# Optimization experiments

Hardware: AMD Instinct MI355X
Metric: run time of the kernel (lower is better)

Reference implementation:

```python
import jax, jax.numpy as jnp
import numpy as np

B, T, C, H = 4, 2048, 1024, 16
HD = C // H  # head_dim = 64


def setup_inputs() -> dict:
    key = jax.random.key(0)
    k1, k2, k3 = jax.random.split(key, 3)
    x = jax.random.normal(k1, (B, T, C), dtype=jnp.float32)
    # nn.Linear weights are [out, in]; we store transposed [in, out] for x @ W
    w_qkv = jax.random.normal(k2, (C, 3 * C), dtype=jnp.float32) * (1.0 / np.sqrt(C))
    w_proj = jax.random.normal(k3, (C, C), dtype=jnp.float32) * (1.0 / np.sqrt(C))
    return {"x": x, "w_qkv": w_qkv, "w_proj": w_proj}


def reference(x, w_qkv, w_proj):
    Bs, Ts, Cs = x.shape
    qkv = x @ w_qkv  # [B,T,3C]
    q, k, v = jnp.split(qkv, 3, axis=-1)

    def split_heads(t):
        return t.reshape(Bs, Ts, H, HD).transpose(0, 2, 1, 3)  # [B,H,T,HD]

    q, k, v = split_heads(q), split_heads(k), split_heads(v)
    scale = 1.0 / np.sqrt(HD)
    scores = jnp.einsum('bhqd,bhkd->bhqk', q, k) * scale  # [B,H,T,T]
    causal = jnp.tril(jnp.ones((Ts, Ts), dtype=bool))
    scores = jnp.where(causal, scores, -jnp.inf)
    weights = jax.nn.softmax(scores, axis=-1)
    out = jnp.einsum('bhqk,bhkd->bhqd', weights, v)  # [B,H,T,HD]
    out = out.transpose(0, 2, 1, 3).reshape(Bs, Ts, Cs)
    return out @ w_proj
```

## Files before the change

kernel.cpp:

```cpp
#include <hip/hip_runtime.h>
#include <stdint.h>


typedef __attribute__((ext_vector_type(8))) short bf16x8;
typedef __attribute__((ext_vector_type(4))) float f32x4;

#define MFMA(a, b, c) __builtin_amdgcn_mfma_f32_16x16x32_bf16((a), (b), (c), 0, 0, 0)

#define NB 4
#define NT 2048
#define NC 1024
#define NH 16
#define HD 64
#define SCALE_Q 0.18033688011112042f

__device__ __forceinline__ short f2bf(float f) {
  union { float fv; uint32_t u; } v; v.fv = f;
  uint32_t u = v.u;
  uint32_t r = (u + 0x7fffu + ((u >> 16) & 1u)) >> 16;
  return (short)(r & 0xffffu);
}

__device__ __forceinline__ uint32_t pkbf(float a, float b) {
  union { float f; uint32_t u; } ua, ub; ua.f = a; ub.f = b;
  return __builtin_amdgcn_perm(ub.u + 0x8000u, ua.u + 0x8000u, 0x07060302u);
}

__device__ __forceinline__ void gl_lds16(const void* g, void* l) {
  __builtin_amdgcn_global_load_lds(
      (const __attribute__((address_space(1))) void*)g,
      (__attribute__((address_space(3))) void*)l, 16, 0, 0);
}


__global__ void cast_f32_bf16(const float* __restrict__ src, short* __restrict__ dst, int n8) {
  int i = blockIdx.x * blockDim.x + threadIdx.x;
  if (i >= n8) return;
  const float4* s4 = (const float4*)src;
  float4 a = s4[2 * i], b = s4[2 * i + 1];
  bf16x8 o;
  o[0] = f2bf(a.x); o[1] = f2bf(a.y); o[2] = f2bf(a.z); o[3] = f2bf(a.w);
  o[4] = f2bf(b.x); o[5] = f2bf(b.y); o[6] = f2bf(b.z); o[7] = f2bf(b.w);
  *(bf16x8*)&dst[8 * i] = o;
}

__global__ void transpose_cast(const float* __restrict__ src, short* __restrict__ dst,
                               int R, int Cc) {
  __shared__ float tile[64][65];
  int tid = threadIdx.x;
  int c0 = blockIdx.x * 64;
  int r0 = blockIdx.y * 64;
  int lr = tid >> 4;
  int lc = (tid & 15) * 4;
#pragma unroll
  for (int i = 0; i < 4; i++) {
    int rr = lr + i * 16;
    float4 v = *(const float4*)&src[(size_t)(r0 + rr) * Cc + c0 + lc];
    tile[rr][lc + 0] = v.x; tile[rr][lc + 1] = v.y;
    tile[rr][lc + 2] = v.z; tile[rr][lc + 3] = v.w;
  }
  __syncthreads();
  int oc = tid >> 2;
  int seg = (tid & 3) * 16;
  bf16x8 o0, o1;
#pragma unroll
  for (int u = 0; u < 8; u++) o0[u] = f2bf(tile[seg + u][oc]);
#pragma unroll
  for (int u = 0; u < 8; u++) o1[u] = f2bf(tile[seg + 8 + u][oc]);
  size_t base = (size_t)(c0 + oc) * R + r0 + seg;
  *(bf16x8*)&dst[base] = o0;
  *(bf16x8*)&dst[base + 8] = o1;
}


__global__ __launch_bounds__(256, 2)
void gemm_bt_kernel(const short* __restrict__ A, const short* __restrict__ BT,
                    int N, int K, int nbx, int mode,
                    short* __restrict__ q, short* __restrict__ kk, short* __restrict__ vT,
                    float* __restrict__ f_out) {
  __shared__ short sA[128 * 64];
  __shared__ short sB[128 * 64];
  const int tid = threadIdx.x;
  const int lane = tid & 63;
  const int w = tid >> 6;
  const int quad = lane >> 4;
  const int r = lane & 15;

  const int bid = blockIdx.x;
  const int xcd = bid & 7;
  const int local = bid >> 3;
  const int mloc = local / nbx, nloc = local - mloc * nbx;
  const int bm0 = (xcd * 8 + mloc) * 128;
  const int bn0 = nloc * 128;

  const int wm = (w >> 1) * 64;
  const int wn = (w & 1) * 64;
  const int sel = (mode == 0) ? (bn0 >> 10) : 3;
  const bool swapped = (sel != 2);

  f32x4 acc[4][4];
#pragma unroll
  for (int i = 0; i < 4; i++)
#pragma unroll
    for (int j = 0; j < 4; j++) acc[i][j] = (f32x4){0.f, 0.f, 0.f, 0.f};

  for (int kb = 0; kb < K; kb += 64) {
    __syncthreads();
#pragma unroll
    for (int j2 = 0; j2 < 4; j2++) {
      int idx = (w * 4 + j2) * 64 + lane;
      int row = idx >> 3, ch = idx & 7;
      int g = ch ^ (row & 7);
      gl_lds16(A + (size_t)(bm0 + row) * K + kb + g * 8, (char*)sA + idx * 16);
      gl_lds16(BT + (size_t)(bn0 + row) * K + kb + g * 8, (char*)sB + idx * 16);
    }
    __syncthreads();
#pragma unroll
    for (int c = 0; c < 2; c++) {
      bf16x8 af[4], bfr[4];
#pragma unroll
      for (int i = 0; i < 4; i++) {
        const int sw = ((c << 2) + quad) ^ (r & 7);
        af[i]  = *(const bf16x8*)&sA[(wm + i * 16 + r) * 64 + sw * 8];
        bfr[i] = *(const bf16x8*)&sB[(wn + i * 16 + r) * 64 + sw * 8];
      }
      if (swapped) {
#pragma unroll
        for (int i = 0; i < 4; i++)
#pragma unroll
          for (int j = 0; j < 4; j++)
            acc[i][j] = MFMA(bfr[j], af[i], acc[i][j]);
      } else {
#pragma unroll
        for (int i = 0; i < 4; i++)
#pragma unroll
          for (int j = 0; j < 4; j++)
            acc[i][j] = MFMA(af[i], bfr[j], acc[i][j]);
      }
    }
  }

  if (mode == 1) {
#pragma unroll
    for (int i = 0; i < 4; i++) {
      const int m = bm0 + wm + i * 16 + r;
#pragma unroll
      for (int j = 0; j < 4; j++) {
        const int nf = bn0 + wn + j * 16 + quad * 4;
        *(f32x4*)&f_out[(size_t)m * N + nf] = acc[i][j];
      }
    }
  } else if (sel == 2) {
#pragma unroll
    for (int j = 0; j < 4; j++) {
      const int n = bn0 + wn + j * 16 + r;
      const int d = n & 63, h = (n & 1023) >> 6;
#pragma unroll
      for (int i = 0; i < 4; i++) {
        const int t0 = bm0 + wm + i * 16 + quad * 4;
        const int bh = (t0 >> 11) * NH + h;
        uint2 pk = make_uint2(pkbf(acc[i][j][0], acc[i][j][1]),
                              pkbf(acc[i][j][2], acc[i][j][3]));
        *(uint2*)&vT[((size_t)bh * HD + d) * NT + (t0 & 2047)] = pk;
      }
    }
  } else {
    short* dst = (sel == 0) ? q : kk;
    const float scl = (sel == 0) ? SCALE_Q : 1.0f;
#pragma unroll
    for (int i = 0; i < 4; i++) {
      const int t = bm0 + wm + i * 16 + r;
      const int bb = (t >> 11) * NH;
      const int tt = t & 2047;
#pragma unroll
      for (int j = 0; j < 4; j++) {
        const int nf = bn0 + wn + j * 16 + quad * 4;
        const int rem = nf & 1023, h = rem >> 6, d0 = rem & 63;
        uint2 pk = make_uint2(pkbf(acc[i][j][0] * scl, acc[i][j][1] * scl),
                              pkbf(acc[i][j][2] * scl, acc[i][j][3] * scl));
        *(uint2*)&dst[((size_t)(bb + h) * NT + tt) * HD + d0] = pk;
      }
    }
  }
}


__device__ __forceinline__ void attn_band(
    const short* __restrict__ Qb, const short* __restrict__ Kb,
    const short* __restrict__ VTb, short* __restrict__ Og,
    short* __restrict__ sK, short* __restrict__ sV, short* __restrict__ sPw,
    const int band, const int bh, const int w, const int lane) {
  const int quad = lane >> 4;
  const int r = lane & 15;
  const int q0 = band * 128 + w * 32;

  bf16x8 bQ[2][2];
#pragma unroll
  for (int mi = 0; mi < 2; mi++) {
    const size_t qrow = ((size_t)q0 + mi * 16 + r) * HD;
    bQ[mi][0] = *(const bf16x8*)&Qb[qrow + quad * 8];
    bQ[mi][1] = *(const bf16x8*)&Qb[qrow + 32 + quad * 8];
  }
  bf16x8 vone;
#pragma unroll
  for (int u = 0; u < 8; u++) vone[u] = (short)0x3F80;

  f32x4 acc[2][4];
  f32x4 lacc[2];
#pragma unroll
  for (int mi = 0; mi < 2; mi++) {
    lacc[mi] = (f32x4){0.f, 0.f, 0.f, 0.f};
#pragma unroll
    for (int dt = 0; dt < 4; dt++) acc[mi][dt] = (f32x4){0.f, 0.f, 0.f, 0.f};
  }

  for (int kt = 0; kt <= band; kt++) {
    const int kv0 = kt * 128;
    const bool diag = (kt == band);
    __syncthreads();
#pragma unroll
    for (int j = 0; j < 4; j++) {
      int idx = (w * 4 + j) * 64 + lane;
      int krow = idx >> 3, kch = idx & 7;
      int kg = kch ^ (krow & 7);
      gl_lds16(Kb + (size_t)(kv0 + krow) * HD + kg * 8, (char*)sK + idx * 16);
      int vrow = idx >> 4, vch = idx & 15;
      int vg = (vch & 8) | ((vch ^ vrow) & 7);
      gl_lds16(VTb + (size_t)vrow * NT + kv0 + vg * 8, (char*)sV + idx * 16);
    }
    __syncthreads();

    bf16x8 vf[4][4];
#pragma unroll
    for (int dt = 0; dt < 4; dt++)
#pragma unroll
      for (int c = 0; c < 4; c++) {
        int ch = quad + 4 * c;
        int sw = (ch & 8) | ((ch ^ (r & 7)) & 7);
        vf[dt][c] = *(const bf16x8*)&sV[(dt * 16 + r) * 128 + sw * 8];
      }

#pragma unroll
    for (int mi = 0; mi < 2; mi++) {
      const int nts = diag ? (w * 2 + mi + 1) : 8;
#pragma unroll
      for (int nt = 0; nt < 8; nt++) {
        uint2 pk = make_uint2(0u, 0u);
        if (nt < nts) {
          const int krow = nt * 16 + r;
          const int sw0 = quad ^ (r & 7);
          bf16x8 k0 = *(const bf16x8*)&sK[krow * 64 + sw0 * 8];
          bf16x8 k1 = *(const bf16x8*)&sK[krow * 64 + (sw0 ^ 4) * 8];
          f32x4 st = (f32x4){0.f, 0.f, 0.f, 0.f};
          st = MFMA(k0, bQ[mi][0], st);
          st = MFMA(k1, bQ[mi][1], st);
          if (diag && nt == nts - 1) {
            const int kvb = kv0 + nt * 16 + quad * 4;
            const int qg = q0 + mi * 16 + r;
#pragma unroll
            for (int reg = 0; reg < 4; reg++)
              if (kvb + reg > qg) st[reg] = -1e30f;
          }
          pk.x = pkbf(__builtin_amdgcn_exp2f(st[0]), __builtin_amdgcn_exp2f(st[1]));
          pk.y = pkbf(__builtin_amdgcn_exp2f(st[2]), __builtin_amdgcn_exp2f(st[3]));
        }
        *(uint2*)&sPw[r * 136 + nt * 16 + quad * 4] = pk;
      }
      __builtin_amdgcn_s_waitcnt(0xc07f);
      bf16x8 aP[4];
#pragma unroll
      for (int c = 0; c < 4; c++)
        aP[c] = *(const bf16x8*)&sPw[r * 136 + c * 32 + quad * 8];
#pragma unroll
      for (int c = 0; c < 4; c++)
        lacc[mi] = MFMA(aP[c], vone, lacc[mi]);
#pragma unroll
      for (int dt = 0; dt < 4; dt++)
#pragma unroll
        for (int c = 0; c < 4; c++)
          acc[mi][dt] = MFMA(aP[c], vf[dt][c], acc[mi][dt]);
    }
  }

  const int b = bh >> 4, h = bh & 15;
#pragma unroll
  for (int mi = 0; mi < 2; mi++)
#pragma unroll
    for (int reg = 0; reg < 4; reg++) {
      const int trow = q0 + mi * 16 + quad * 4 + reg;
      const float inv = 1.0f / lacc[mi][reg];
      const size_t base = ((size_t)(b * NT + trow)) * NC + h * HD;
#pragma unroll
      for (int dt = 0; dt < 4; dt++)
        Og[base + dt * 16 + r] = f2bf(acc[mi][dt][reg] * inv);
    }
}

__global__ __launch_bounds__(256, 3)
void attn_kernel(const short* __restrict__ Q, const short* __restrict__ Kg,
                 const short* __restrict__ VT, short* __restrict__ Og) {
  __shared__ short sK[128 * 64];
  __shared__ short sV[64 * 128];
  __shared__ short sP[4][16 * 136];
  const int tid = threadIdx.x;
  const int lane = tid & 63;
  const int w = tid >> 6;

  const int n = blockIdx.x;
  const int xcd = n & 7;
  const int slot = n >> 3;
  const int bh = xcd * 8 + (slot & 7);
  const int pr = slot >> 3;

  const short* Qb  = Q  + (size_t)bh * NT * HD;
  const short* Kb  = Kg + (size_t)bh * NT * HD;
  const short* VTb = VT + (size_t)bh * HD * NT;

  attn_band(Qb, Kb, VTb, Og, sK, sV, &sP[w][0], 15 - pr, bh, w, lane);
  attn_band(Qb, Kb, VTb, Og, sK, sV, &sP[w][0], pr, bh, w, lane);
}


extern "C" void kernel_launch(void* const* d_in, const int* in_sizes, int n_in,
                              void* d_out, int out_size, void* d_ws, size_t ws_size,
                              hipStream_t stream) {
  const float* x     = (const float*)d_in[0];
  const float* wqkv  = (const float*)d_in[1];
  const float* wproj = (const float*)d_in[2];
  float* out = (float*)d_out;

  char* ws = (char*)d_ws;
  short* xb  = (short*)(ws + 0);
  short* wqT = (short*)(ws + 16777216);
  short* wpT = (short*)(ws + 23068672);
  short* q   = (short*)(ws + 25165824);
  short* kk  = (short*)(ws + 41943040);
  short* vT  = (short*)(ws + 58720256);
  short* att = (short*)(ws + 75497472);

  cast_f32_bf16<<<4096, 256, 0, stream>>>(x, xb, (NB * NT * NC) / 8);
  transpose_cast<<<dim3(48, 16), 256, 0, stream>>>(wqkv, wqT, NC, 3 * NC);
  transpose_cast<<<dim3(16, 16), 256, 0, stream>>>(wproj, wpT, NC, NC);
  gemm_bt_kernel<<<1536, 256, 0, stream>>>(xb, wqT, 3 * NC, NC, 24, 0, q, kk, vT, nullptr);
  attn_kernel<<<512, 256, 0, stream>>>(q, kk, vT, att);
  gemm_bt_kernel<<<512, 256, 0, stream>>>(att, wpT, NC, NC, 8, 1, nullptr, nullptr, nullptr, out);
}
```

Baseline: 300.0 us.

## Launch one attention block per causal band and share K fragment loads across row tiles

The attention grid goes from 512 blocks, each doing a paired heavy and light causal band, to 1024 blocks that each do a single band. Heavy bands are dispatched first so the hardware scheduler can balance the uneven causal work. Inside each KV tile, the two 16-row query sub-tiles now share a single set of K fragment loads from LDS. The second sub-tile's packed probabilities are held in registers until the first sub-tile's PV MFMAs finish. This trims LDS reads and adds parallelism, at the cost of more register pressure and less explicit pairing of work per block.

Measured after the change: 274.7 us. -8.4%, faster.

```diff
diff --git a/kernel.cpp b/kernel.cpp
--- a/kernel.cpp
+++ b/kernel.cpp
@@ -240,45 +240,81 @@
         vf[dt][c] = *(const bf16x8*)&sV[(dt * 16 + r) * 128 + sw * 8];
       }
 
-#pragma unroll
-    for (int mi = 0; mi < 2; mi++) {
-      const int nts = diag ? (w * 2 + mi + 1) : 8;
-#pragma unroll
-      for (int nt = 0; nt < 8; nt++) {
-        uint2 pk = make_uint2(0u, 0u);
-        if (nt < nts) {
-          const int krow = nt * 16 + r;
-          const int sw0 = quad ^ (r & 7);
-          bf16x8 k0 = *(const bf16x8*)&sK[krow * 64 + sw0 * 8];
-          bf16x8 k1 = *(const bf16x8*)&sK[krow * 64 + (sw0 ^ 4) * 8];
+    const int nts0 = diag ? (w * 2 + 1) : 8;
+    const int nts1 = diag ? (w * 2 + 2) : 8;
+    uint2 pk1r[8];
+#pragma unroll
+    for (int nt = 0; nt < 8; nt++) {
+      uint2 pk0 = make_uint2(0u, 0u);
+      pk1r[nt] = make_uint2(0u, 0u);
+      if (nt < nts1) {
+        const int krow = nt * 16 + r;
+        const int sw0 = quad ^ (r & 7);
+        bf16x8 k0 = *(const bf16x8*)&sK[krow * 64 + sw0 * 8];
+        bf16x8 k1 = *(const bf16x8*)&sK[krow * 64 + (sw0 ^ 4) * 8];
+        if (nt < nts0) {
           f32x4 st = (f32x4){0.f, 0.f, 0.f, 0.f};
-          st = MFMA(k0, bQ[mi][0], st);
-          st = MFMA(k1, bQ[mi][1], st);
-          if (diag && nt == nts - 1) {
+          st = MFMA(k0, bQ[0][0], st);
+          st = MFMA(k1, bQ[0][1], st);
+          if (diag && nt == nts0 - 1) {
             const int kvb = kv0 + nt * 16 + quad * 4;
-            const int qg = q0 + mi * 16 + r;
+            const int qg = q0 + r;
 #pragma unroll
             for (int reg = 0; reg < 4; reg++)
               if (kvb + reg > qg) st[reg] = -1e30f;
           }
-          pk.x = pkbf(__builtin_amdgcn_exp2f(st[0]), __builtin_amdgcn_exp2f(st[1]));
-          pk.y = pkbf(__builtin_amdgcn_exp2f(st[2]), __builtin_amdgcn_exp2f(st[3]));
+          pk0.x = pkbf(__builtin_amdgcn_exp2f(st[0]), __builtin_amdgcn_exp2f(st[1]));
+          pk0.y = pkbf(__builtin_amdgcn_exp2f(st[2]), __builtin_amdgcn_exp2f(st[3]));
         }
-        *(uint2*)&sPw[r * 136 + nt * 16 + quad * 4] = pk;
-      }
-      __builtin_amdgcn_s_waitcnt(0xc07f);
+        {
+          f32x4 st = (f32x4){0.f, 0.f, 0.f, 0.f};
+          st = MFMA(k0, bQ[1][0], st);
+          st = MFMA(k1, bQ[1][1], st);
+          if (diag && nt == nts1 - 1) {
+            const int kvb = kv0 + nt * 16 + quad * 4;
+            const int qg = q0 + 16 + r;
+#pragma unroll
+            for (int reg = 0; reg < 4; reg++)
+              if (kvb + reg > qg) st[reg] = -1e30f;
+          }
+          pk1r[nt].x = pkbf(__builtin_amdgcn_exp2f(st[0]), __builtin_amdgcn_exp2f(st[1]));
+          pk1r[nt].y = pkbf(__builtin_amdgcn_exp2f(st[2]), __builtin_amdgcn_exp2f(st[3]));
+        }
+      }
+      *(uint2*)&sPw[r * 136 + nt * 16 + quad * 4] = pk0;
+    }
+    __builtin_amdgcn_s_waitcnt(0xc07f);
+    {
       bf16x8 aP[4];
 #pragma unroll
       for (int c = 0; c < 4; c++)
         aP[c] = *(const bf16x8*)&sPw[r * 136 + c * 32 + quad * 8];
 #pragma unroll
       for (int c = 0; c < 4; c++)
-        lacc[mi] = MFMA(aP[c], vone, lacc[mi]);
+        lacc[0] = MFMA(aP[c], vone, lacc[0]);
 #pragma unroll
       for (int dt = 0; dt < 4; dt++)
 #pragma unroll
         for (int c = 0; c < 4; c++)
-          acc[mi][dt] = MFMA(aP[c], vf[dt][c], acc[mi][dt]);
+          acc[0][dt] = MFMA(aP[c], vf[dt][c], acc[0][dt]);
+    }
+#pragma unroll
+    for (int nt = 0; nt < 8; nt++)
+      *(uint2*)&sPw[r * 136 + nt * 16 + quad * 4] = pk1r[nt];
+    __builtin_amdgcn_s_waitcnt(0xc07f);
+    {
+      bf16x8 aP[4];
+#pragma unroll
+      for (int c = 0; c < 4; c++)
+        aP[c] = *(const bf16x8*)&sPw[r * 136 + c * 32 + quad * 8];
+#pragma unroll
+      for (int c = 0; c < 4; c++)
+        lacc[1] = MFMA(aP[c], vone, lacc[1]);
+#pragma unroll
+      for (int dt = 0; dt < 4; dt++)
+#pragma unroll
+        for (int c = 0; c < 4; c++)
+          acc[1][dt] = MFMA(aP[c], vf[dt][c], acc[1][dt]);
     }
   }
 
@@ -310,14 +346,13 @@
   const int xcd = n & 7;
   const int slot = n >> 3;
   const int bh = xcd * 8 + (slot & 7);
-  const int pr = slot >> 3;
+  const int band = 15 - (slot >> 3);
 
   const short* Qb  = Q  + (size_t)bh * NT * HD;
   const short* Kb  = Kg + (size_t)bh * NT * HD;
   const short* VTb = VT + (size_t)bh * HD * NT;
 
-  attn_band(Qb, Kb, VTb, Og, sK, sV, &sP[w][0], 15 - pr, bh, w, lane);
-  attn_band(Qb, Kb, VTb, Og, sK, sV, &sP[w][0], pr, bh, w, lane);
+  attn_band(Qb, Kb, VTb, Og, sK, sV, &sP[w][0], band, bh, w, lane);
 }
 
 
@@ -342,6 +377,6 @@
   transpose_cast<<<dim3(48, 16), 256, 0, stream>>>(wqkv, wqT, NC, 3 * NC);
   transpose_cast<<<dim3(16, 16), 256, 0, stream>>>(wproj, wpT, NC, NC);
   gemm_bt_kernel<<<1536, 256, 0, stream>>>(xb, wqT, 3 * NC, NC, 24, 0, q, kk, vT, nullptr);
-  attn_kernel<<<512, 256, 0, stream>>>(q, kk, vT, att);
+  attn_kernel<<<1024, 256, 0, stream>>>(q, kk, vT, att);
   gemm_bt_kernel<<<512, 256, 0, stream>>>(att, wpT, NC, NC, 8, 1, nullptr, nullptr, nullptr, out);
 }
```
